# Kernel tuning notes

Hardware: AMD Instinct MI355X
Metric: run time of the kernel (lower is better)

## Reference

```python
import jax, jax.numpy as jnp
import numpy as np

I, H, L, O = 11, 33, 3, 18

def lstm_layer(x_tbi, W_ih, W_hh, b_ih, b_hh):
    # x_tbi: [T, B, in]; W_ih: [4H, in]; W_hh: [4H, H]
    T, B = x_tbi.shape[0], x_tbi.shape[1]
    # precompute input contribution for all timesteps (one big GEMM)
    xg = jnp.einsum('tbi,gi->tbg', x_tbi, W_ih) + b_ih + b_hh  # [T, B, 4H]
    h0 = jnp.zeros((B, H), x_tbi.dtype)
    c0 = jnp.zeros((B, H), x_tbi.dtype)

    def step(carry, xg_t):
        h, c = carry
        gates = xg_t + h @ W_hh.T                      # [B, 4H]
        i, f, g, o = jnp.split(gates, 4, axis=-1)      # PyTorch gate order i,f,g,o
        i = jax.nn.sigmoid(i)
        f = jax.nn.sigmoid(f)
        g = jnp.tanh(g)
        o = jax.nn.sigmoid(o)
        c = f * c + i * g
        h = o * jnp.tanh(c)
        return (h, c), h

    (hT, cT), ys = jax.lax.scan(step, (h0, c0), xg)
    return ys, hT, cT  # ys: [T, B, H]


def setup_inputs() -> dict:
    key = jax.random.key(0)
    ks = jax.random.split(key, 20)
    B, T = 512, 2048
    s = 1.0 / np.sqrt(H)
    d = {'x': jax.random.normal(ks[0], (B, T, I), jnp.float32)}
    in_sizes = [I, H, H]
    for l in range(L):
        d[f'W_ih{l}'] = jax.random.uniform(ks[1 + 4 * l], (4 * H, in_sizes[l]), jnp.float32, -s, s)
        d[f'W_hh{l}'] = jax.random.uniform(ks[2 + 4 * l], (4 * H, H), jnp.float32, -s, s)
        d[f'b_ih{l}'] = jax.random.uniform(ks[3 + 4 * l], (4 * H,), jnp.float32, -s, s)
        d[f'b_hh{l}'] = jax.random.uniform(ks[4 + 4 * l], (4 * H,), jnp.float32, -s, s)
    d['W1'] = jax.random.normal(ks[13], (4 * O, H), jnp.float32) * 0.05
    d['b1'] = jnp.zeros((4 * O,), jnp.float32)
    d['W2'] = jax.random.normal(ks[14], (O, 4 * O), jnp.float32) * 0.05
    d['b2'] = jnp.zeros((O,), jnp.float32)
    return d


def reference(x, W_ih0, W_hh0, b_ih0, b_hh0, W_ih1, W_hh1, b_ih1, b_hh1,
              W_ih2, W_hh2, b_ih2, b_hh2, W1, b1, W2, b2):
    # x: [B, T, I] (batch_first) -> time-major for scan
    xt = jnp.transpose(x, (1, 0, 2))  # [T, B, I]
    params = [(W_ih0, W_hh0, b_ih0, b_hh0),
              (W_ih1, W_hh1, b_ih1, b_hh1),
              (W_ih2, W_hh2, b_ih2, b_hh2)]
    hiddens = []
    cur = xt
    for (Wi, Wh, bi, bh) in params:
        cur, hT, _ = lstm_layer(cur, Wi, Wh, bi, bh)
        hiddens.append(hT)
    hidden = jnp.stack(hiddens, axis=0)  # [L, B, H] (final hidden state per layer)
    # MLP head (dropout inactive at inference); torch nn.GELU default = exact erf
    h1 = jax.nn.gelu(hidden @ W1.T + b1, approximate=False)
    out = h1 @ W2.T + b2  # [L, B, O]
    return out, hidden
```

## Files before the change

### kernel.cpp

```cpp
#include <hip/hip_runtime.h>
#include <math.h>

#define TT 2048
#define BB 512
#define II 11
#define HH 33
#define NL 3
#define OO 18
#define FSLOT 40

typedef float f2 __attribute__((ext_vector_type(2)));

__device__ __forceinline__ float sigm_f(float x) {
    float e = __expf(-x);
    return __builtin_amdgcn_rcpf(1.0f + e);
}
__device__ __forceinline__ float tanh_f(float x) {
    float e = __expf(2.0f * x);
    return 1.0f - 2.0f * __builtin_amdgcn_rcpf(e + 1.0f);
}

__device__ __forceinline__ float dppx1(float v) {
    return __int_as_float(__builtin_amdgcn_update_dpp(
        0, __float_as_int(v), 0xB1 , 0xF, 0xF, true));
}

#define PK(acc, w, v) asm("v_pk_fma_f32 %0, %1, %2, %0" : "+v"(acc) : "v"(w), "v"(v))

__global__ __launch_bounds__(256, 1) void lstm_pipeline_kernel(
    const float* __restrict__ x,
    const float* __restrict__ Wih0, const float* __restrict__ Whh0,
    const float* __restrict__ bih0, const float* __restrict__ bhh0,
    const float* __restrict__ Wih1, const float* __restrict__ Whh1,
    const float* __restrict__ bih1, const float* __restrict__ bhh1,
    const float* __restrict__ Wih2, const float* __restrict__ Whh2,
    const float* __restrict__ bih2, const float* __restrict__ bhh2,
    const float* __restrict__ W1, const float* __restrict__ b1,
    const float* __restrict__ W2, const float* __restrict__ b2,
    float* __restrict__ hidden_out,
    float* __restrict__ outp)
{
    __shared__ __align__(16) float buf[2][NL + 1][FSLOT];
    __shared__ float hfin[NL][HH + 1];
    __shared__ float h1s[NL][4 * OO];

    const int tid = threadIdx.x;
    const int bg  = blockIdx.x;

    for (int i = tid; i < 2 * (NL + 1) * FSLOT; i += 256)
        ((float*)buf)[i] = 0.0f;

    const bool comp = (tid < 2 * 99);
    const int  u    = tid >> 1;
    const int  hf   = tid & 1;
    const int  l    = (u < 33) ? 0 : (u < 66) ? 1 : 2;
    const int  j    = u - 33 * l;
    const int  koff = hf ? 16 : 0;

    const int  pi   = tid - 200;
    const bool pref = (pi >= 0) && (pi < II);
    const int  pic  = pref ? pi : 0;
    const float* xrow = x + (size_t)bg * TT * II + pic;

    f2 wI[4][9], wH[4][9];
    #pragma unroll
    for (int g = 0; g < 4; ++g) {
        #pragma unroll
        for (int r = 0; r < 9; ++r) { wI[g][r] = (f2){0.f, 0.f}; wH[g][r] = (f2){0.f, 0.f}; }
    }
    float b0 = 0.0f, b1v = 0.0f, b2v = 0.0f, b3v = 0.0f;

    if (comp) {
        if (!hf) {
            const float* bip = (l == 0) ? bih0 : (l == 1) ? bih1 : bih2;
            const float* bhp = (l == 0) ? bhh0 : (l == 1) ? bhh1 : bhh2;
            b0  = bip[0 * HH + j] + bhp[0 * HH + j];
            b1v = bip[1 * HH + j] + bhp[1 * HH + j];
            b2v = bip[2 * HH + j] + bhp[2 * HH + j];
            b3v = bip[3 * HH + j] + bhp[3 * HH + j];
        }
        const float* Wi = (l == 0) ? Wih0 : (l == 1) ? Wih1 : Wih2;
        const float* Wh = (l == 0) ? Whh0 : (l == 1) ? Whh1 : Whh2;
        const int kin = (l == 0) ? II : HH;
        #pragma unroll
        for (int g = 0; g < 4; ++g) {
            const float* rw = Wi + (g * HH + j) * kin;
            const float* rh = Wh + (g * HH + j) * HH;
            #pragma unroll
            for (int r = 0; r < 9; ++r) {
                const int  k    = koff + 2 * r;
                const bool dead = (!hf) && (r == 8);
                wI[g][r].x = (!dead && k     < kin) ? rw[k]     : 0.0f;
                wI[g][r].y = (!dead && k + 1 < kin) ? rw[k + 1] : 0.0f;
                wH[g][r].x = (!dead && k     < HH)  ? rh[k]     : 0.0f;
                wH[g][r].y = (!dead && k + 1 < HH)  ? rh[k + 1] : 0.0f;
            }
        }
    }

    const float kX = hf ? 2.0f : -1.0f;
    const float AX = hf ? 1.0f : 0.0f;
    const float BX = hf ? -2.0f : 1.0f;

    __syncthreads();
    float v_next = 0.0f, v_next2 = 0.0f;
    if (pref) {
        buf[0][0][pi] = xrow[0];
        v_next  = xrow[II];
        v_next2 = xrow[2 * II];
    }
    __syncthreads();

    float c = 0.0f;

    const float* rin[2]  = { &buf[0][l][0],     &buf[1][l][0] };
    const float* rown[2] = { &buf[0][l + 1][0], &buf[1][l + 1][0] };
    float*       wrp[2]  = { &buf[0][l + 1][j], &buf[1][l + 1][j] };
    float*       pxp[2]  = { &buf[0][0][pic],   &buf[1][0][pic] };

    auto step = [&](int s, int rp, bool check, bool out, bool xload, bool xstore)
        __attribute__((always_inline)) {
        const int wp = rp ^ 1;
        if (pref) {
            if (xstore) *pxp[wp] = v_next;
            v_next = v_next2;
            if (xload) v_next2 = xrow[(size_t)(s + 3) * II];
        }
        const bool active = check ? (comp && (s >= l) && (s - l < TT)) : comp;
        if (active) {
            const float* ri = rin[rp];
            const float* ro = rown[rp];
            f2 vi[9], vo[9];
            #pragma unroll
            for (int r = 0; r < 9; ++r) {
                vi[r] = *(const f2*)(ri + koff + 2 * r);
                vo[r] = *(const f2*)(ro + koff + 2 * r);
            }

            f2 a0 = {b0, 0.0f}, a1 = {b1v, 0.0f}, a2 = {b2v, 0.0f}, a3 = {b3v, 0.0f};
            #pragma unroll
            for (int r = 0; r < 9; ++r) {
                PK(a0, wI[0][r], vi[r]); PK(a1, wI[1][r], vi[r]);
                PK(a2, wI[2][r], vi[r]); PK(a3, wI[3][r], vi[r]);
            }
            #pragma unroll
            for (int r = 0; r < 9; ++r) {
                PK(a0, wH[0][r], vo[r]); PK(a1, wH[1][r], vo[r]);
                PK(a2, wH[2][r], vo[r]); PK(a3, wH[3][r], vo[r]);
            }

            float s0 = a0.x + a0.y, s1 = a1.x + a1.y;
            float s2 = a2.x + a2.y, s3 = a3.x + a3.y;
            s0 += dppx1(s0); s1 += dppx1(s1);
            s2 += dppx1(s2); s3 += dppx1(s3);

            const float aXv = hf ? s2 : s0;
            const float eX  = __expf(kX * aXv);
            const float rX  = __builtin_amdgcn_rcpf(1.0f + eX);
            const float xg  = __builtin_fmaf(BX, rX, AX);
            const float yg  = sigm_f(hf ? s3 : s1);

            const float xp = dppx1(xg);
            const float yp = dppx1(yg);
            const float ig = hf ? xp : xg;
            const float fg = hf ? yp : yg;
            const float gg = hf ? xg : xp;
            const float og = hf ? yg : yp;

            c = __builtin_fmaf(fg, c, ig * gg);
            const float hnew = og * tanh_f(c);

            if (!hf) {
                *wrp[wp] = hnew;
                if (out && (s - l == TT - 1)) {
                    hidden_out[((size_t)l * BB + bg) * HH + j] = hnew;
                    hfin[l][j] = hnew;
                }
            }
        }
        __syncthreads();
    };

    step(0, 0, true, false, true, true);
    step(1, 1, true, false, true, true);
    for (int s = 2; s < TT - 4; s += 2) {
        step(s,     0, false, false, true, true);
        step(s + 1, 1, false, false, true, true);
    }
    step(TT - 4, 0, false, false, true,  true);
    step(TT - 3, 1, false, false, false, true);
    step(TT - 2, 0, false, false, false, true);
    step(TT - 1, 1, false, true,  false, false);
    step(TT,     0, true,  true,  false, false);
    step(TT + 1, 1, true,  true,  false, false);

    if (tid < 4 * OO) {
        #pragma unroll
        for (int ml = 0; ml < NL; ++ml) {
            float a = b1[tid];
            #pragma unroll
            for (int k = 0; k < HH; ++k) a += hfin[ml][k] * W1[tid * HH + k];
            h1s[ml][tid] = 0.5f * a * (1.0f + erff(a * 0.70710678118654752f));
        }
    }
    __syncthreads();
    if (tid < NL * OO) {
        const int ol = tid / OO, o = tid % OO;
        float a = b2[o];
        #pragma unroll
        for (int m = 0; m < 4 * OO; ++m) a += h1s[ol][m] * W2[o * (4 * OO) + m];
        outp[((size_t)ol * BB + bg) * OO + o] = a;
    }
}

extern "C" void kernel_launch(void* const* d_in, const int* in_sizes, int n_in,
                              void* d_out, int out_size, void* d_ws, size_t ws_size,
                              hipStream_t stream) {
    const float* x    = (const float*)d_in[0];
    const float* Wih0 = (const float*)d_in[1];
    const float* Whh0 = (const float*)d_in[2];
    const float* bih0 = (const float*)d_in[3];
    const float* bhh0 = (const float*)d_in[4];
    const float* Wih1 = (const float*)d_in[5];
    const float* Whh1 = (const float*)d_in[6];
    const float* bih1 = (const float*)d_in[7];
    const float* bhh1 = (const float*)d_in[8];
    const float* Wih2 = (const float*)d_in[9];
    const float* Whh2 = (const float*)d_in[10];
    const float* bih2 = (const float*)d_in[11];
    const float* bhh2 = (const float*)d_in[12];
    const float* W1   = (const float*)d_in[13];
    const float* b1   = (const float*)d_in[14];
    const float* W2   = (const float*)d_in[15];
    const float* b2   = (const float*)d_in[16];

    float* out    = (float*)d_out;
    float* hidden = out + NL * BB * OO;

    lstm_pipeline_kernel<<<BB, 256, 0, stream>>>(
        x, Wih0, Whh0, bih0, bhh0, Wih1, Whh1, bih1, bhh1,
        Wih2, Whh2, bih2, bhh2, W1, b1, W2, b2, hidden, out);
}
```

Measured before the change: 1.244 ms.

## Allow two blocks per CU and switch to scalar FMAs with vector LDS loads

```diff
diff --git a/kernel.cpp b/kernel.cpp
--- a/kernel.cpp
+++ b/kernel.cpp
@@ -10,6 +10,7 @@
 #define FSLOT 40
 
 typedef float f2 __attribute__((ext_vector_type(2)));
+typedef float f4 __attribute__((ext_vector_type(4)));
 
 __device__ __forceinline__ float sigm_f(float x) {
     float e = __expf(-x);
@@ -25,9 +26,7 @@
         0, __float_as_int(v), 0xB1 , 0xF, 0xF, true));
 }
 
-#define PK(acc, w, v) asm("v_pk_fma_f32 %0, %1, %2, %0" : "+v"(acc) : "v"(w), "v"(v))
-
-__global__ __launch_bounds__(256, 1) void lstm_pipeline_kernel(
+__global__ __launch_bounds__(256, 2) void lstm_pipeline_kernel(
     const float* __restrict__ x,
     const float* __restrict__ Wih0, const float* __restrict__ Whh0,
     const float* __restrict__ bih0, const float* __restrict__ bhh0,
@@ -62,12 +61,11 @@
     const int  pic  = pref ? pi : 0;
     const float* xrow = x + (size_t)bg * TT * II + pic;
 
-    f2 wI[4][9], wH[4][9];
+    float wI[4][18], wH[4][18];
     #pragma unroll
-    for (int g = 0; g < 4; ++g) {
-        #pragma unroll
-        for (int r = 0; r < 9; ++r) { wI[g][r] = (f2){0.f, 0.f}; wH[g][r] = (f2){0.f, 0.f}; }
-    }
+    for (int g = 0; g < 4; ++g)
+        #pragma unroll
+        for (int r = 0; r < 18; ++r) { wI[g][r] = 0.0f; wH[g][r] = 0.0f; }
     float b0 = 0.0f, b1v = 0.0f, b2v = 0.0f, b3v = 0.0f;
 
     if (comp) {
@@ -87,13 +85,11 @@
             const float* rw = Wi + (g * HH + j) * kin;
             const float* rh = Wh + (g * HH + j) * HH;
             #pragma unroll
-            for (int r = 0; r < 9; ++r) {
-                const int  k    = koff + 2 * r;
-                const bool dead = (!hf) && (r == 8);
-                wI[g][r].x = (!dead && k     < kin) ? rw[k]     : 0.0f;
-                wI[g][r].y = (!dead && k + 1 < kin) ? rw[k + 1] : 0.0f;
-                wH[g][r].x = (!dead && k     < HH)  ? rh[k]     : 0.0f;
-                wH[g][r].y = (!dead && k + 1 < HH)  ? rh[k + 1] : 0.0f;
+            for (int r = 0; r < 18; ++r) {
+                const int  k    = koff + r;
+                const bool own  = hf ? true : (r < 16);
+                wI[g][r] = (own && k < kin) ? rw[k] : 0.0f;
+                wH[g][r] = (own && k < HH)  ? rh[k] : 0.0f;
             }
         }
     }
@@ -128,29 +124,35 @@
         }
         const bool active = check ? (comp && (s >= l) && (s - l < TT)) : comp;
         if (active) {
-            const float* ri = rin[rp];
-            const float* ro = rown[rp];
-            f2 vi[9], vo[9];
-            #pragma unroll
-            for (int r = 0; r < 9; ++r) {
-                vi[r] = *(const f2*)(ri + koff + 2 * r);
-                vo[r] = *(const f2*)(ro + koff + 2 * r);
-            }
-
-            f2 a0 = {b0, 0.0f}, a1 = {b1v, 0.0f}, a2 = {b2v, 0.0f}, a3 = {b3v, 0.0f};
-            #pragma unroll
-            for (int r = 0; r < 9; ++r) {
-                PK(a0, wI[0][r], vi[r]); PK(a1, wI[1][r], vi[r]);
-                PK(a2, wI[2][r], vi[r]); PK(a3, wI[3][r], vi[r]);
-            }
-            #pragma unroll
-            for (int r = 0; r < 9; ++r) {
-                PK(a0, wH[0][r], vo[r]); PK(a1, wH[1][r], vo[r]);
-                PK(a2, wH[2][r], vo[r]); PK(a3, wH[3][r], vo[r]);
-            }
-
-            float s0 = a0.x + a0.y, s1 = a1.x + a1.y;
-            float s2 = a2.x + a2.y, s3 = a3.x + a3.y;
+            const float* ri = rin[rp] + koff;
+            const float* ro = rown[rp] + koff;
+            float vi[18], vo[18];
+            #pragma unroll
+            for (int q = 0; q < 4; ++q) {
+                const f4 a = *(const f4*)(ri + 4 * q);
+                const f4 b = *(const f4*)(ro + 4 * q);
+                vi[4 * q + 0] = a.x; vi[4 * q + 1] = a.y; vi[4 * q + 2] = a.z; vi[4 * q + 3] = a.w;
+                vo[4 * q + 0] = b.x; vo[4 * q + 1] = b.y; vo[4 * q + 2] = b.z; vo[4 * q + 3] = b.w;
+            }
+            { const f2 a = *(const f2*)(ri + 16); vi[16] = a.x; vi[17] = a.y;
+              const f2 b = *(const f2*)(ro + 16); vo[16] = b.x; vo[17] = b.y; }
+
+            float s0 = b0, s1 = b1v, s2 = b2v, s3 = b3v;
+            #pragma unroll
+            for (int r = 0; r < 18; ++r) {
+                s0 = __builtin_fmaf(wI[0][r], vi[r], s0);
+                s1 = __builtin_fmaf(wI[1][r], vi[r], s1);
+                s2 = __builtin_fmaf(wI[2][r], vi[r], s2);
+                s3 = __builtin_fmaf(wI[3][r], vi[r], s3);
+            }
+            #pragma unroll
+            for (int r = 0; r < 18; ++r) {
+                s0 = __builtin_fmaf(wH[0][r], vo[r], s0);
+                s1 = __builtin_fmaf(wH[1][r], vo[r], s1);
+                s2 = __builtin_fmaf(wH[2][r], vo[r], s2);
+                s3 = __builtin_fmaf(wH[3][r], vo[r], s3);
+            }
+
             s0 += dppx1(s0); s1 += dppx1(s1);
             s2 += dppx1(s2); s3 += dppx1(s3);
 
@@ -160,15 +162,10 @@
             const float xg  = __builtin_fmaf(BX, rX, AX);
             const float yg  = sigm_f(hf ? s3 : s1);
 
-            const float xp = dppx1(xg);
-            const float yp = dppx1(yg);
-            const float ig = hf ? xp : xg;
-            const float fg = hf ? yp : yg;
-            const float gg = hf ? xg : xp;
-            const float og = hf ? yg : yp;
-
-            c = __builtin_fmaf(fg, c, ig * gg);
-            const float hnew = og * tanh_f(c);
+            const float prod = xg * dppx1(xg);
+            const float yp   = dppx1(yg);
+            c = __builtin_fmaf(yg, c, prod);
+            const float hnew = yp * tanh_f(c);
 
             if (!hf) {
                 *wrp[wp] = hnew;
```

After: 1.319 ms. 6.1% more time.
